# Kernel tuning notes

Measured on AMD Instinct MI355X. Metric: run time of the kernel, lower is better.

Reference implementation:

```python
import jax, jax.numpy as jnp
import numpy as np

B, S, H = 64, 512, 768
N_SPANS, MAX_SPAN, CW = 4, 8, 3
NH = 8
HD = H // NH
W = MAX_SPAN + 1 + 2 * CW  # max context window length (15)
H2 = H // 2
N_ATE, N_SENT = 2, 2


def _ln(x, g, b, eps=1e-5):
    m = x.mean(-1, keepdims=True)
    v = ((x - m) ** 2).mean(-1, keepdims=True)
    return (x - m) / jnp.sqrt(v + eps) * g + b


def _classifier(x, w1, b1, g, bb, w2, b2):
    # Dropout -> Linear -> GELU -> LayerNorm -> Linear (eval mode: dropout = id)
    h = jax.nn.gelu(x @ w1.T + b1, approximate=False)
    h = _ln(h, g, bb)
    return h @ w2.T + b2


def setup_inputs() -> dict:
    key = jax.random.key(0)
    ks = jax.random.split(key, 16)
    p = lambda k, shape: (0.02 * jax.random.normal(k, shape)).astype(jnp.float32)
    seq_out = jax.random.normal(ks[0], (B, S, H), dtype=jnp.float32)
    starts = jax.random.randint(ks[1], (B, N_SPANS), 1, S - MAX_SPAN - 1)
    lens = jax.random.randint(ks[2], (B, N_SPANS), 1, MAX_SPAN + 1)
    ends = starts + lens  # exclusive end, span length in [1, MAX_SPAN]
    return dict(
        seq_out=seq_out,
        span_starts=starts.astype(jnp.int32),
        span_ends=ends.astype(jnp.int32),
        ate_g=jnp.ones((H,), jnp.float32), ate_b=jnp.zeros((H,), jnp.float32),
        apc_g=jnp.ones((H,), jnp.float32), apc_b=jnp.zeros((H,), jnp.float32),
        w_in=p(ks[3], (3 * H, H)), b_in=jnp.zeros((3 * H,), jnp.float32),
        w_out=p(ks[4], (H, H)), b_out=jnp.zeros((H,), jnp.float32),
        fus_w=p(ks[5], (H, 2 * H)), fus_b=jnp.zeros((H,), jnp.float32),
        asp_w1=p(ks[6], (H2, H)), asp_b1=jnp.zeros((H2,), jnp.float32),
        asp_lng=jnp.ones((H2,), jnp.float32), asp_lnb=jnp.zeros((H2,), jnp.float32),
        asp_w2=p(ks[7], (N_ATE, H2)), asp_b2=jnp.zeros((N_ATE,), jnp.float32),
        sen_w1=p(ks[8], (H2, H)), sen_b1=jnp.zeros((H2,), jnp.float32),
        sen_lng=jnp.ones((H2,), jnp.float32), sen_lnb=jnp.zeros((H2,), jnp.float32),
        sen_w2=p(ks[9], (N_SENT, H2)), sen_b2=jnp.zeros((N_SENT,), jnp.float32),
    )


def _fwd(seq_out, ate_g, ate_b, apc_g, apc_b, w_in, b_in, w_out, b_out,
         fus_w, fus_b, asp_w1, asp_b1, asp_lng, asp_lnb, asp_w2, asp_b2,
         sen_w1, sen_b1, sen_lng, sen_lnb, sen_w2, sen_b2,
         span_starts, span_ends):
    dt = seq_out.dtype
    # clamping semantics as in the torch loop
    s = jnp.clip(span_starts, 0, S - 1)
    e = jnp.maximum(s, jnp.minimum(span_ends, S - 1))
    left = jnp.maximum(0, s - CW)
    right = jnp.minimum(S, e + 1 + CW)

    # ATE head over all tokens
    ate_logits = _classifier(_ln(seq_out, ate_g, ate_b),
                             asp_w1, asp_b1, asp_lng, asp_lnb, asp_w2, asp_b2)

    gather = jax.vmap(lambda so, idx: so[idx])  # ([S,H],[N,W]) -> [N,W,H]

    # aspect mean over tokens [s, e)
    aidx = s[..., None] + jnp.arange(MAX_SPAN)          # [B,N,MS]
    va = (aidx < e[..., None]).astype(dt)
    asp_tok = gather(seq_out, jnp.clip(aidx, 0, S - 1)) # [B,N,MS,H]
    cnt = va.sum(-1, keepdims=True)                     # [B,N,1]
    asp_mean = (asp_tok * va[..., None]).sum(-2) / jnp.maximum(cnt, 1.0)
    asp_mean = jnp.where(cnt > 0, asp_mean, seq_out[:, None, 0, :])

    # context window [left, right): tiny self-attention, then mean
    cidx = left[..., None] + jnp.arange(W)              # [B,N,W]
    vc = (cidx < right[..., None]).astype(dt)
    ctx = gather(seq_out, jnp.clip(cidx, 0, S - 1))     # [B,N,W,H]
    qkv = ctx @ w_in.T + b_in
    q, k, v = jnp.split(qkv, 3, axis=-1)
    q = q.reshape(B, N_SPANS, W, NH, HD) * (HD ** -0.5)
    k = k.reshape(B, N_SPANS, W, NH, HD)
    v = v.reshape(B, N_SPANS, W, NH, HD)
    scores = jnp.einsum('bnqhd,bnkhd->bnhqk', q, k)
    neg = jnp.asarray(jnp.finfo(dt).min, dt)
    scores = jnp.where(vc[:, :, None, None, :] > 0, scores, neg)
    attn = jax.nn.softmax(scores, axis=-1)
    out = jnp.einsum('bnhqk,bnkhd->bnqhd', attn, v).reshape(B, N_SPANS, W, H)
    out = out @ w_out.T + b_out
    ccnt = vc.sum(-1, keepdims=True)
    ctx_mean = (out * vc[..., None]).sum(-2) / jnp.maximum(ccnt, 1.0)

    combined = jnp.concatenate([asp_mean, ctx_mean], axis=-1)  # [B,N,2H]
    fused = jax.nn.gelu(combined @ fus_w.T + fus_b, approximate=False)
    apc_feat = fused.mean(axis=1)                              # [B,H]
    apc_logits = _classifier(_ln(apc_feat, apc_g, apc_b),
                             sen_w1, sen_b1, sen_lng, sen_lnb, sen_w2, sen_b2)
    return ate_logits, apc_logits


def reference(seq_out, span_starts, span_ends, ate_g, ate_b, apc_g, apc_b,
              w_in, b_in, w_out, b_out, fus_w, fus_b,
              asp_w1, asp_b1, asp_lng, asp_lnb, asp_w2, asp_b2,
              sen_w1, sen_b1, sen_lng, sen_lnb, sen_w2, sen_b2):
    return _fwd(seq_out, ate_g, ate_b, apc_g, apc_b, w_in, b_in, w_out, b_out,
                fus_w, fus_b, asp_w1, asp_b1, asp_lng, asp_lnb, asp_w2, asp_b2,
                sen_w1, sen_b1, sen_lng, sen_lnb, sen_w2, sen_b2,
                span_starts, span_ends)
```

## Files before the change

kernel.cpp:

```cpp
#include <hip/hip_runtime.h>
#include <math.h>

#define DEVI __device__ __forceinline__

using bf16x8 = __attribute__((ext_vector_type(8))) short;
using f32x4  = __attribute__((ext_vector_type(4))) float;

DEVI float b2f(unsigned short u) {
  union { unsigned int u; float f; } x; x.u = ((unsigned int)u) << 16; return x.f;
}
DEVI unsigned short f2b(float f) {
  union { float f; unsigned int u; } x; x.f = f;
  unsigned int r = (x.u + 0x7fffu + ((x.u >> 16) & 1u)) >> 16;
  return (unsigned short)r;
}
DEVI float gelu_f(float x) { return 0.5f * x * (1.0f + erff(x * 0.70710678118654752440f)); }

DEVI void wredxor2(float& a, float& b) {
  #pragma unroll
  for (int off = 32; off; off >>= 1) {
    a += __shfl_xor(a, off);
    b += __shfl_xor(b, off);
  }
}

template<int NW>
DEVI void breduce2(float& a, float& b) {
  __shared__ float buf[2 * NW];
  int lane = threadIdx.x & 63;
  int w = threadIdx.x >> 6;
  #pragma unroll
  for (int off = 32; off > 0; off >>= 1) {
    a += __shfl_down(a, off);
    b += __shfl_down(b, off);
  }
  if (lane == 0) { buf[w] = a; buf[NW + w] = b; }
  __syncthreads();
  float ra = 0.f, rb = 0.f;
  #pragma unroll
  for (int i = 0; i < NW; ++i) { ra += buf[i]; rb += buf[NW + i]; }
  a = ra; b = rb;
  __syncthreads();
}

DEVI void span_params(const int* st, const int* en, int span,
                      int& s, int& e, int& left, int& right) {
  int s0 = st[span], e0 = en[span];
  s = min(max(s0, 0), 511);
  e = max(s, min(e0, 511));
  left = max(0, s - 3);
  right = min(512, e + 4);
}

DEVI int xcd_logical(int bid, int n) {
  int q = n >> 3, r = n & 7;
  int xcd = bid & 7, idx = bid >> 3;
  return (xcd < r ? xcd * (q + 1) : r * (q + 1) + (xcd - r) * q) + idx;
}

__global__ __launch_bounds__(256) void prep_kernel(
    const float* __restrict__ s0, const float* __restrict__ s1,
    const float* __restrict__ s2, const float* __restrict__ s3,
    const float* __restrict__ s4,
    unsigned short* __restrict__ d0, unsigned short* __restrict__ d1,
    unsigned short* __restrict__ d2, unsigned short* __restrict__ d3,
    unsigned short* __restrict__ d4,
    const float* __restrict__ seq, const float* __restrict__ ate_g,
    const float* __restrict__ ate_b, unsigned short* __restrict__ lnx,
    const int* __restrict__ st, const int* __restrict__ en,
    unsigned short* __restrict__ ctxA) {
  const int bid = blockIdx.x, tid = threadIdx.x;
  if (bid < 4032) {
    int i = bid * 256 + tid;
    const float* s; unsigned short* d; int j;
    if (i < 73728)       { s = s0; d = d0; j = i; }
    else if (i < 516096) { s = s1; d = d1; j = i - 73728; }
    else if (i < 663552) { s = s2; d = d2; j = i - 516096; }
    else if (i < 958464) { s = s3; d = d3; j = i - 663552; }
    else                 { s = s4; d = d4; j = i - 958464; }
    float4 v = reinterpret_cast<const float4*>(s)[j];
    ushort4 o;
    o.x = f2b(v.x); o.y = f2b(v.y); o.z = f2b(v.z); o.w = f2b(v.w);
    reinterpret_cast<ushort4*>(d)[j] = o;
  } else if (bid < 12224) {
    const int row = (bid - 4032) * 4 + (tid >> 6);
    const int lane = tid & 63;
    const float4* xr = reinterpret_cast<const float4*>(seq + (size_t)row * 768);
    float4 v[3];
    #pragma unroll
    for (int j = 0; j < 3; ++j) v[j] = xr[j * 64 + lane];
    float s = 0.f, q = 0.f;
    #pragma unroll
    for (int j = 0; j < 3; ++j) {
      s += v[j].x + v[j].y + v[j].z + v[j].w;
      q += v[j].x * v[j].x + v[j].y * v[j].y + v[j].z * v[j].z + v[j].w * v[j].w;
    }
    wredxor2(s, q);
    float mean = s * (1.0f / 768.0f);
    float rstd = rsqrtf(q * (1.0f / 768.0f) - mean * mean + 1e-5f);
    ushort4* orow = reinterpret_cast<ushort4*>(lnx + (size_t)row * 768);
    #pragma unroll
    for (int j = 0; j < 3; ++j) {
      float4 gv = reinterpret_cast<const float4*>(ate_g)[j * 64 + lane];
      float4 bv = reinterpret_cast<const float4*>(ate_b)[j * 64 + lane];
      ushort4 o;
      o.x = f2b((v[j].x - mean) * rstd * gv.x + bv.x);
      o.y = f2b((v[j].y - mean) * rstd * gv.y + bv.y);
      o.z = f2b((v[j].z - mean) * rstd * gv.z + bv.z);
      o.w = f2b((v[j].w - mean) * rstd * gv.w + bv.w);
      orow[j * 64 + lane] = o;
    }
  } else {
    if (tid >= 192) return;
    int r = bid - 12224;
    int span = r / 15, w = r % 15;
    int s, e, left, right;
    span_params(st, en, span, s, e, left, right);
    int b = span >> 2;
    int tok = min(left + w, 511);
    const float4* src = reinterpret_cast<const float4*>(seq + ((size_t)b * 512 + tok) * 768);
    ushort4* dst = reinterpret_cast<ushort4*>(ctxA + (size_t)r * 768);
    float4 v = src[tid];
    ushort4 o;
    o.x = f2b(v.x); o.y = f2b(v.y); o.z = f2b(v.z); o.w = f2b(v.w);
    dst[tid] = o;
  }
}

template<int BM, int BN, int WM, int WN>
DEVI void gemm_body64(const unsigned short* __restrict__ A,
                      const unsigned short* __restrict__ W,
                      const float* __restrict__ bias, unsigned short* __restrict__ C,
                      int M, int N, int K, bool act, int bm, int bn,
                      unsigned short* As, unsigned short* Bs) {
  constexpr int CA = BM / 8;
  constexpr int CB = BN / 8;
  constexpr int NWC = BN / WN;
  constexpr int WAVES = (BM / WM) * NWC;
  constexpr int FM = WM / 16, FN = WN / 16;
  const int tid = threadIdx.x;
  const int lane = tid & 63;
  const int wv = tid >> 6;
  const int wr = wv / NWC, wc = wv % NWC;
  const int l16 = lane & 15, lhi = lane >> 4;
  const int srow = lane >> 3;
  const int scol = 8 * ((lane & 7) ^ srow);

  f32x4 acc[FM][FN] = {};
  const int nt = K / 64;

  for (int t = 0; t < nt; ++t) {
    const int k0 = t * 64;
    #pragma unroll
    for (int ch = wv; ch < CA; ch += WAVES)
      __builtin_amdgcn_global_load_lds(
          (const __attribute__((address_space(1))) void*)&A[(size_t)(bm + ch * 8 + srow) * K + k0 + scol],
          (__attribute__((address_space(3))) void*)&As[ch * 512], 16, 0, 0);
    #pragma unroll
    for (int ch = wv; ch < CB; ch += WAVES)
      __builtin_amdgcn_global_load_lds(
          (const __attribute__((address_space(1))) void*)&W[(size_t)(bn + ch * 8 + srow) * K + k0 + scol],
          (__attribute__((address_space(3))) void*)&Bs[ch * 512], 16, 0, 0);
    __syncthreads();
    #pragma unroll
    for (int kk = 0; kk < 2; ++kk) {
      bf16x8 af[FM], bfr[FN];
      #pragma unroll
      for (int fm = 0; fm < FM; ++fm) {
        int r = wr * WM + fm * 16 + l16;
        af[fm] = *reinterpret_cast<const bf16x8*>(&As[r * 64 + ((kk * 32 + lhi * 8) ^ ((r & 7) * 8))]);
      }
      #pragma unroll
      for (int fn = 0; fn < FN; ++fn) {
        int r = wc * WN + fn * 16 + l16;
        bfr[fn] = *reinterpret_cast<const bf16x8*>(&Bs[r * 64 + ((kk * 32 + lhi * 8) ^ ((r & 7) * 8))]);
      }
      #pragma unroll
      for (int fm = 0; fm < FM; ++fm)
        #pragma unroll
        for (int fn = 0; fn < FN; ++fn)
          acc[fm][fn] = __builtin_amdgcn_mfma_f32_16x16x32_bf16(af[fm], bfr[fn], acc[fm][fn], 0, 0, 0);
    }
    __syncthreads();
  }

  #pragma unroll
  for (int fm = 0; fm < FM; ++fm) {
    #pragma unroll
    for (int fn = 0; fn < FN; ++fn) {
      int col = bn + wc * WN + fn * 16 + l16;
      float bv = bias[col];
      #pragma unroll
      for (int i = 0; i < 4; ++i) {
        int row = bm + wr * WM + fm * 16 + lhi * 4 + i;
        float v = acc[fm][fn][i] + bv;
        if (act) v = gelu_f(v);
        C[(size_t)row * N + col] = f2b(v);
      }
    }
  }
}

template<int BM, int BN, int WM, int WN, int ACT>
__global__ __launch_bounds__(256) void gemm_swz64(
    const unsigned short* __restrict__ A, const unsigned short* __restrict__ W,
    const float* __restrict__ bias, unsigned short* __restrict__ C,
    int M, int N, int K, int nbN) {
  __shared__ __align__(16) unsigned short As[BM * 64];
  __shared__ __align__(16) unsigned short Bs[BN * 64];
  int l = xcd_logical(blockIdx.x, gridDim.x);
  int mb = l / nbN, nb = l % nbN;
  gemm_body64<BM, BN, WM, WN>(A, W, bias, C, M, N, K, ACT != 0,
                              mb * BM, nb * BN, As, Bs);
}

__global__ __launch_bounds__(512) void dual_gemm_kernel(
    const unsigned short* __restrict__ lnx, const unsigned short* __restrict__ w1b,
    const float* __restrict__ b1, unsigned short* __restrict__ hate,
    const unsigned short* __restrict__ ctxA, const unsigned short* __restrict__ winb,
    const float* __restrict__ b_in, unsigned short* __restrict__ qkv) {
  __shared__ __align__(16) unsigned short lds[384 * 64];
  if (blockIdx.x < 384) {
    int l = xcd_logical(blockIdx.x, 384);
    int mb = l / 3, nb = l % 3;
    gemm_body64<256, 128, 64, 64>(lnx, w1b, b1, hate, 32768, 384, 768, true,
                                  mb * 256, nb * 128, lds, lds + 256 * 64);
  } else {
    int bid = blockIdx.x - 384;
    int l = xcd_logical(bid, 270);
    int mb = l / 9, nb = l % 9;
    gemm_body64<128, 256, 64, 64>(ctxA, winb, b_in, qkv, 3840, 2304, 768, false,
                                  mb * 128, nb * 256, lds, lds + 128 * 64);
  }
}

__global__ __launch_bounds__(256) void finattn_kernel(
    const unsigned short* __restrict__ h, const float* __restrict__ lng,
    const float* __restrict__ lnb, const float* __restrict__ w2,
    const float* __restrict__ b2, float* __restrict__ out,
    const unsigned short* __restrict__ qkv, const int* __restrict__ st,
    const int* __restrict__ en, unsigned short* __restrict__ ctxO) {
  __shared__ float qs[15][96], ks[15][96], vs[15][96];
  __shared__ float sc[15][16];
  const int tid = threadIdx.x;
  if (blockIdx.x < 8192) {
    const int row = blockIdx.x * 4 + (tid >> 6);
    const int lane = tid & 63;
    const unsigned short* hr = h + (size_t)row * 384 + lane * 6;
    ushort2 u0 = *reinterpret_cast<const ushort2*>(hr);
    ushort2 u1 = *reinterpret_cast<const ushort2*>(hr + 2);
    ushort2 u2 = *reinterpret_cast<const ushort2*>(hr + 4);
    float v[6] = { b2f(u0.x), b2f(u0.y), b2f(u1.x), b2f(u1.y), b2f(u2.x), b2f(u2.y) };
    float s = 0.f, q = 0.f;
    #pragma unroll
    for (int j = 0; j < 6; ++j) { s += v[j]; q += v[j] * v[j]; }
    wredxor2(s, q);
    float mean = s * (1.f / 384.f);
    float rstd = rsqrtf(q * (1.f / 384.f) - mean * mean + 1e-5f);
    const int c0 = lane * 6;
    float p0 = 0.f, p1 = 0.f;
    #pragma unroll
    for (int j = 0; j < 6; ++j) {
      float hl = (v[j] - mean) * rstd * lng[c0 + j] + lnb[c0 + j];
      p0 += hl * w2[c0 + j];
      p1 += hl * w2[384 + c0 + j];
    }
    wredxor2(p0, p1);
    if (lane == 0) {
      out[(size_t)row * 2]     = p0 + b2[0];
      out[(size_t)row * 2 + 1] = p1 + b2[1];
    }
    return;
  }
  const int blk = blockIdx.x - 8192;
  const int span = blk >> 3, hh = blk & 7;
  int s, e, left, right;
  span_params(st, en, span, s, e, left, right);
  const int nv = right - left;
  const int r0 = span * 15;
  const float scale = 0.10206207261596576f;
  if (tid < 180) {
    int w = tid / 12, dp = tid % 12, d = dp * 8;
    const unsigned short* rowp = qkv + (size_t)(r0 + w) * 2304 + hh * 96 + d;
    bf16x8 qv = *reinterpret_cast<const bf16x8*>(rowp);
    bf16x8 kv = *reinterpret_cast<const bf16x8*>(rowp + 768);
    bf16x8 vv = *reinterpret_cast<const bf16x8*>(rowp + 1536);
    #pragma unroll
    for (int j = 0; j < 8; ++j) {
      qs[w][d + j] = b2f((unsigned short)qv[j]) * scale;
      ks[w][d + j] = b2f((unsigned short)kv[j]);
      vs[w][d + j] = b2f((unsigned short)vv[j]);
    }
  }
  __syncthreads();
  if (tid < 225) {
    int i = tid / 15, j = tid % 15;
    float a = 0.f;
    #pragma unroll
    for (int d = 0; d < 96; ++d) a += qs[i][d] * ks[j][d];
    sc[i][j] = (j < nv) ? a : -3.402823466e38f;
  }
  __syncthreads();
  if (tid < 15) {
    int i = tid;
    float m = -3.402823466e38f;
    #pragma unroll
    for (int j = 0; j < 15; ++j) m = fmaxf(m, sc[i][j]);
    float ex[15];
    float ssum = 0.f;
    #pragma unroll
    for (int j = 0; j < 15; ++j) { ex[j] = expf(sc[i][j] - m); ssum += ex[j]; }
    float inv = 1.0f / ssum;
    #pragma unroll
    for (int j = 0; j < 15; ++j) sc[i][j] = ex[j] * inv;
  }
  __syncthreads();
  for (int idx = tid; idx < 720; idx += 256) {
    int w = idx / 48, dp = idx % 48, d = dp * 2;
    float o0 = 0.f, o1 = 0.f;
    #pragma unroll
    for (int j = 0; j < 15; ++j) {
      float p = sc[w][j];
      o0 += p * vs[j][d];
      o1 += p * vs[j][d + 1];
    }
    ushort2 o; o.x = f2b(o0); o.y = f2b(o1);
    *reinterpret_cast<ushort2*>(&ctxO[(size_t)(r0 + w) * 768 + hh * 96 + d]) = o;
  }
}

__global__ __launch_bounds__(256) void means_kernel(
    const float* __restrict__ seq, const unsigned short* __restrict__ projO,
    const int* __restrict__ st, const int* __restrict__ en,
    unsigned short* __restrict__ comb) {
  const int span = blockIdx.x;
  int s, e, left, right;
  span_params(st, en, span, s, e, left, right);
  int b = span >> 2;
  int e2 = min(e, s + 8);
  int cnt = e2 - s;
  int nv = right - left;
  float inva = (cnt > 0) ? 1.0f / (float)cnt : 0.f;
  float invc = 1.0f / (float)nv;
  for (int c = threadIdx.x; c < 768; c += 256) {
    float sa = 0.f;
    for (int t = s; t < e2; ++t) sa += seq[((size_t)b * 512 + t) * 768 + c];
    float asp = (cnt > 0) ? sa * inva : seq[((size_t)b * 512) * 768 + c];
    comb[(size_t)span * 1536 + c] = f2b(asp);
    float sc_ = 0.f;
    for (int w = 0; w < nv; ++w) sc_ += b2f(projO[(size_t)(span * 15 + w) * 768 + c]);
    comb[(size_t)span * 1536 + 768 + c] = f2b(sc_ * invc);
  }
}

__global__ __launch_bounds__(256) void apc_all_kernel(
    const unsigned short* __restrict__ fused, const float* __restrict__ g,
    const float* __restrict__ bb, const unsigned short* __restrict__ senb,
    const float* __restrict__ b1, const float* __restrict__ lng,
    const float* __restrict__ lnb, const float* __restrict__ w2,
    const float* __restrict__ b2, float* __restrict__ out) {
  const int b = blockIdx.x, tid = threadIdx.x;
  __shared__ float xs[768];
  __shared__ float hs[384];
  float v[3];
  #pragma unroll
  for (int j = 0; j < 3; ++j) {
    int c = tid + j * 256;
    float a = 0.f;
    #pragma unroll
    for (int n = 0; n < 4; ++n) a += b2f(fused[((size_t)(b * 4 + n)) * 768 + c]);
    v[j] = 0.25f * a;
  }
  float s = v[0] + v[1] + v[2];
  float q = v[0] * v[0] + v[1] * v[1] + v[2] * v[2];
  breduce2<4>(s, q);
  float mean = s * (1.f / 768.f);
  float rstd = rsqrtf(q * (1.f / 768.f) - mean * mean + 1e-5f);
  #pragma unroll
  for (int j = 0; j < 3; ++j) {
    int c = tid + j * 256;
    xs[c] = (v[j] - mean) * rstd * g[c] + bb[c];
  }
  __syncthreads();
  for (int j = tid; j < 384; j += 256) {
    const bf16x8* wrp = reinterpret_cast<const bf16x8*>(senb + (size_t)j * 768);
    float dot = 0.f;
    #pragma unroll 4
    for (int k8 = 0; k8 < 96; ++k8) {
      bf16x8 wv = wrp[k8];
      #pragma unroll
      for (int u = 0; u < 8; ++u) dot += xs[k8 * 8 + u] * b2f((unsigned short)wv[u]);
    }
    hs[j] = gelu_f(dot + b1[j]);
  }
  __syncthreads();
  s = 0.f; q = 0.f;
  for (int j = tid; j < 384; j += 256) { float h = hs[j]; s += h; q += h * h; }
  breduce2<4>(s, q);
  mean = s * (1.f / 384.f);
  rstd = rsqrtf(q * (1.f / 384.f) - mean * mean + 1e-5f);
  float p0 = 0.f, p1 = 0.f;
  for (int j = tid; j < 384; j += 256) {
    float hl = (hs[j] - mean) * rstd * lng[j] + lnb[j];
    p0 += hl * w2[j];
    p1 += hl * w2[384 + j];
  }
  breduce2<4>(p0, p1);
  if (tid == 0) {
    out[b * 2]     = p0 + b2[0];
    out[b * 2 + 1] = p1 + b2[1];
  }
}

extern "C" void kernel_launch(void* const* d_in, const int* in_sizes, int n_in,
                              void* d_out, int out_size, void* d_ws, size_t ws_size,
                              hipStream_t stream) {
  const float* seq    = (const float*)d_in[0];
  const int*   st     = (const int*)d_in[1];
  const int*   en     = (const int*)d_in[2];
  const float* ate_g  = (const float*)d_in[3];
  const float* ate_b  = (const float*)d_in[4];
  const float* apc_g  = (const float*)d_in[5];
  const float* apc_b  = (const float*)d_in[6];
  const float* w_in   = (const float*)d_in[7];
  const float* b_in   = (const float*)d_in[8];
  const float* w_out  = (const float*)d_in[9];
  const float* b_out  = (const float*)d_in[10];
  const float* fus_w  = (const float*)d_in[11];
  const float* fus_b  = (const float*)d_in[12];
  const float* asp_w1 = (const float*)d_in[13];
  const float* asp_b1 = (const float*)d_in[14];
  const float* asp_lng= (const float*)d_in[15];
  const float* asp_lnb= (const float*)d_in[16];
  const float* asp_w2 = (const float*)d_in[17];
  const float* asp_b2 = (const float*)d_in[18];
  const float* sen_w1 = (const float*)d_in[19];
  const float* sen_b1 = (const float*)d_in[20];
  const float* sen_lng= (const float*)d_in[21];
  const float* sen_lnb= (const float*)d_in[22];
  const float* sen_w2 = (const float*)d_in[23];
  const float* sen_b2 = (const float*)d_in[24];
  float* out = (float*)d_out;

  char* wsb = (char*)d_ws;
  unsigned short* lnx   = (unsigned short*)(wsb + 0);
  unsigned short* ctxA  = (unsigned short*)(wsb + 52428800);
  unsigned short* qkvb  = (unsigned short*)(wsb + 58720256);
  unsigned short* ctxO  = (unsigned short*)(wsb + 77594624);
  unsigned short* projO = (unsigned short*)(wsb + 83886080);
  unsigned short* comb  = (unsigned short*)(wsb + 89849856);
  unsigned short* fusO  = (unsigned short*)(wsb + 90636288);
  const size_t off_w = 91275264;
  unsigned short* hate  = (unsigned short*)(wsb + off_w);
  const size_t off_w2 = off_w + 25165824;
  unsigned short* w1b   = (unsigned short*)(wsb + off_w2);
  unsigned short* winb  = (unsigned short*)(wsb + off_w2 + 589824);
  unsigned short* woutb = (unsigned short*)(wsb + off_w2 + 4128768);
  unsigned short* fusb  = (unsigned short*)(wsb + off_w2 + 5308416);
  unsigned short* senb  = (unsigned short*)(wsb + off_w2 + 7667712);

  prep_kernel<<<16064, 256, 0, stream>>>(asp_w1, w_in, w_out, fus_w, sen_w1,
                                         w1b, winb, woutb, fusb, senb,
                                         seq, ate_g, ate_b, lnx, st, en, ctxA);
  dual_gemm_kernel<<<654, 512, 0, stream>>>(lnx, w1b, asp_b1, hate,
                                            ctxA, winb, b_in, qkvb);
  finattn_kernel<<<10240, 256, 0, stream>>>(hate, asp_lng, asp_lnb, asp_w2, asp_b2, out,
                                            qkvb, st, en, ctxO);
  gemm_swz64<64, 128, 32, 64, 0><<<360, 256, 0, stream>>>(
      ctxO, woutb, b_out, projO, 3840, 768, 768, 6);
  means_kernel<<<256, 256, 0, stream>>>(seq, projO, st, en, comb);
  gemm_swz64<64, 64, 32, 32, 1><<<48, 256, 0, stream>>>(
      comb, fusb, fus_b, fusO, 256, 768, 1536, 12);
  apc_all_kernel<<<64, 256, 0, stream>>>(fusO, apc_g, apc_b, senb, sen_b1,
                                         sen_lng, sen_lnb, sen_w2, sen_b2, out + 65536);
}
```

Before: 188.0 us.

## Fuse ATE LayerNorm and final projection into first GEMM epilogue via partial sums

The ATE classifier's hidden activations are no longer written out in bf16 and re-read. Instead the GEMM epilogue computes per-row partial sums, sums of squares and gamma-weighted dot products with w2, and stores them as small float4 partials. A light pass in the attention kernel then combines the partials and applies the LayerNorm algebraically to produce the logits. This removes the 32768x384 bf16 intermediate round trip and thousands of reduction blocks. The cost is extra shuffle reductions in the epilogue, plus variance computed as E[h^2]-mu^2 in fp32, which has different rounding.

Result: faster. 183.2 us (-2.5%).

```diff
diff --git a/kernel.cpp b/kernel.cpp
--- a/kernel.cpp
+++ b/kernel.cpp
@@ -128,11 +128,11 @@
 }
 
 template<int BM, int BN, int WM, int WN>
-DEVI void gemm_body64(const unsigned short* __restrict__ A,
-                      const unsigned short* __restrict__ W,
-                      const float* __restrict__ bias, unsigned short* __restrict__ C,
-                      int M, int N, int K, bool act, int bm, int bn,
-                      unsigned short* As, unsigned short* Bs) {
+DEVI void gemm_core(const unsigned short* __restrict__ A,
+                    const unsigned short* __restrict__ W,
+                    int K, int bm, int bn,
+                    unsigned short* As, unsigned short* Bs,
+                    f32x4 (&acc)[WM / 16][WN / 16]) {
   constexpr int CA = BM / 8;
   constexpr int CB = BN / 8;
   constexpr int NWC = BN / WN;
@@ -146,9 +146,7 @@
   const int srow = lane >> 3;
   const int scol = 8 * ((lane & 7) ^ srow);
 
-  f32x4 acc[FM][FN] = {};
   const int nt = K / 64;
-
   for (int t = 0; t < nt; ++t) {
     const int k0 = t * 64;
     #pragma unroll
@@ -183,7 +181,17 @@
     }
     __syncthreads();
   }
-
+}
+
+template<int BM, int BN, int WM, int WN>
+DEVI void gemm_store(const float* __restrict__ bias, unsigned short* __restrict__ C,
+                     int N, bool act, int bm, int bn, f32x4 (&acc)[WM / 16][WN / 16]) {
+  constexpr int NWC = BN / WN;
+  constexpr int FM = WM / 16, FN = WN / 16;
+  const int lane = threadIdx.x & 63;
+  const int wv = threadIdx.x >> 6;
+  const int wr = wv / NWC, wc = wv % NWC;
+  const int l16 = lane & 15, lhi = lane >> 4;
   #pragma unroll
   for (int fm = 0; fm < FM; ++fm) {
     #pragma unroll
@@ -210,70 +218,113 @@
   __shared__ __align__(16) unsigned short Bs[BN * 64];
   int l = xcd_logical(blockIdx.x, gridDim.x);
   int mb = l / nbN, nb = l % nbN;
-  gemm_body64<BM, BN, WM, WN>(A, W, bias, C, M, N, K, ACT != 0,
-                              mb * BM, nb * BN, As, Bs);
+  f32x4 acc[WM / 16][WN / 16] = {};
+  gemm_core<BM, BN, WM, WN>(A, W, K, mb * BM, nb * BN, As, Bs, acc);
+  gemm_store<BM, BN, WM, WN>(bias, C, N, ACT != 0, mb * BM, nb * BN, acc);
 }
 
 __global__ __launch_bounds__(512) void dual_gemm_kernel(
     const unsigned short* __restrict__ lnx, const unsigned short* __restrict__ w1b,
-    const float* __restrict__ b1, unsigned short* __restrict__ hate,
+    const float* __restrict__ b1, const float* __restrict__ lng,
+    const float* __restrict__ w2, float4* __restrict__ hpart,
     const unsigned short* __restrict__ ctxA, const unsigned short* __restrict__ winb,
     const float* __restrict__ b_in, unsigned short* __restrict__ qkv) {
   __shared__ __align__(16) unsigned short lds[384 * 64];
   if (blockIdx.x < 384) {
     int l = xcd_logical(blockIdx.x, 384);
     int mb = l / 3, nb = l % 3;
-    gemm_body64<256, 128, 64, 64>(lnx, w1b, b1, hate, 32768, 384, 768, true,
-                                  mb * 256, nb * 128, lds, lds + 256 * 64);
+    const int bm = mb * 256, bn = nb * 128;
+    f32x4 acc[4][4] = {};
+    gemm_core<256, 128, 64, 64>(lnx, w1b, 768, bm, bn, lds, lds + 256 * 64, acc);
+    const int lane = threadIdx.x & 63;
+    const int wv = threadIdx.x >> 6;
+    const int wr = wv >> 1, wc = wv & 1;
+    const int l16 = lane & 15, lhi = lane >> 4;
+    float b1v[4], gw2a[4], gw2b[4];
+    #pragma unroll
+    for (int fn = 0; fn < 4; ++fn) {
+      int col = bn + wc * 64 + fn * 16 + l16;
+      b1v[fn] = b1[col];
+      float gg = lng[col];
+      gw2a[fn] = gg * w2[col];
+      gw2b[fn] = gg * w2[384 + col];
+    }
+    #pragma unroll
+    for (int fm = 0; fm < 4; ++fm) {
+      #pragma unroll
+      for (int i = 0; i < 4; ++i) {
+        float s1 = 0.f, s2 = 0.f, q0 = 0.f, q1 = 0.f;
+        #pragma unroll
+        for (int fn = 0; fn < 4; ++fn) {
+          float h = gelu_f(acc[fm][fn][i] + b1v[fn]);
+          s1 += h; s2 += h * h;
+          q0 += h * gw2a[fn]; q1 += h * gw2b[fn];
+        }
+        #pragma unroll
+        for (int off = 1; off < 16; off <<= 1) {
+          s1 += __shfl_xor(s1, off); s2 += __shfl_xor(s2, off);
+          q0 += __shfl_xor(q0, off); q1 += __shfl_xor(q1, off);
+        }
+        if (l16 == 0) {
+          int row = bm + wr * 64 + fm * 16 + lhi * 4 + i;
+          hpart[(size_t)row * 6 + nb * 2 + wc] = make_float4(s1, s2, q0, q1);
+        }
+      }
+    }
   } else {
     int bid = blockIdx.x - 384;
     int l = xcd_logical(bid, 270);
     int mb = l / 9, nb = l % 9;
-    gemm_body64<128, 256, 64, 64>(ctxA, winb, b_in, qkv, 3840, 2304, 768, false,
-                                  mb * 128, nb * 256, lds, lds + 128 * 64);
+    f32x4 acc[4][4] = {};
+    gemm_core<128, 256, 64, 64>(ctxA, winb, 768, mb * 128, nb * 256,
+                                lds, lds + 128 * 64, acc);
+    gemm_store<128, 256, 64, 64>(b_in, qkv, 2304, false, mb * 128, nb * 256, acc);
   }
 }
 
 __global__ __launch_bounds__(256) void finattn_kernel(
-    const unsigned short* __restrict__ h, const float* __restrict__ lng,
+    const float4* __restrict__ hpart, const float* __restrict__ lng,
     const float* __restrict__ lnb, const float* __restrict__ w2,
     const float* __restrict__ b2, float* __restrict__ out,
     const unsigned short* __restrict__ qkv, const int* __restrict__ st,
     const int* __restrict__ en, unsigned short* __restrict__ ctxO) {
+  const int tid = threadIdx.x;
+  if (blockIdx.x >= 2048) {
+    __shared__ float cbuf[16];
+    float c1a = 0.f, c1b = 0.f, c2a = 0.f, c2b = 0.f;
+    for (int c = tid; c < 384; c += 256) {
+      float gg = lng[c], bbv = lnb[c], wa = w2[c], wb = w2[384 + c];
+      c1a += gg * wa; c1b += gg * wb;
+      c2a += bbv * wa; c2b += bbv * wb;
+    }
+    wredxor2(c1a, c1b);
+    wredxor2(c2a, c2b);
+    if ((tid & 63) == 0) {
+      int w = tid >> 6;
+      cbuf[w * 4] = c1a; cbuf[w * 4 + 1] = c1b;
+      cbuf[w * 4 + 2] = c2a; cbuf[w * 4 + 3] = c2b;
+    }
+    __syncthreads();
+    c1a = cbuf[0] + cbuf[4] + cbuf[8] + cbuf[12];
+    c1b = cbuf[1] + cbuf[5] + cbuf[9] + cbuf[13];
+    c2a = cbuf[2] + cbuf[6] + cbuf[10] + cbuf[14];
+    c2b = cbuf[3] + cbuf[7] + cbuf[11] + cbuf[15];
+    const int row = (blockIdx.x - 2048) * 256 + tid;
+    float S1 = 0.f, S2 = 0.f, D0 = 0.f, D1 = 0.f;
+    #pragma unroll
+    for (int p = 0; p < 6; ++p) {
+      float4 v = hpart[(size_t)row * 6 + p];
+      S1 += v.x; S2 += v.y; D0 += v.z; D1 += v.w;
+    }
+    float mu = S1 * (1.f / 384.f);
+    float rstd = rsqrtf(S2 * (1.f / 384.f) - mu * mu + 1e-5f);
+    out[(size_t)row * 2]     = rstd * (D0 - mu * c1a) + c2a + b2[0];
+    out[(size_t)row * 2 + 1] = rstd * (D1 - mu * c1b) + c2b + b2[1];
+    return;
+  }
   __shared__ float qs[15][96], ks[15][96], vs[15][96];
   __shared__ float sc[15][16];
-  const int tid = threadIdx.x;
-  if (blockIdx.x < 8192) {
-    const int row = blockIdx.x * 4 + (tid >> 6);
-    const int lane = tid & 63;
-    const unsigned short* hr = h + (size_t)row * 384 + lane * 6;
-    ushort2 u0 = *reinterpret_cast<const ushort2*>(hr);
-    ushort2 u1 = *reinterpret_cast<const ushort2*>(hr + 2);
-    ushort2 u2 = *reinterpret_cast<const ushort2*>(hr + 4);
-    float v[6] = { b2f(u0.x), b2f(u0.y), b2f(u1.x), b2f(u1.y), b2f(u2.x), b2f(u2.y) };
-    float s = 0.f, q = 0.f;
-    #pragma unroll
-    for (int j = 0; j < 6; ++j) { s += v[j]; q += v[j] * v[j]; }
-    wredxor2(s, q);
-    float mean = s * (1.f / 384.f);
-    float rstd = rsqrtf(q * (1.f / 384.f) - mean * mean + 1e-5f);
-    const int c0 = lane * 6;
-    float p0 = 0.f, p1 = 0.f;
-    #pragma unroll
-    for (int j = 0; j < 6; ++j) {
-      float hl = (v[j] - mean) * rstd * lng[c0 + j] + lnb[c0 + j];
-      p0 += hl * w2[c0 + j];
-      p1 += hl * w2[384 + c0 + j];
-    }
-    wredxor2(p0, p1);
-    if (lane == 0) {
-      out[(size_t)row * 2]     = p0 + b2[0];
-      out[(size_t)row * 2 + 1] = p1 + b2[1];
-    }
-    return;
-  }
-  const int blk = blockIdx.x - 8192;
-  const int span = blk >> 3, hh = blk & 7;
+  const int span = blockIdx.x >> 3, hh = blockIdx.x & 7;
   int s, e, left, right;
   span_params(st, en, span, s, e, left, right);
   const int nv = right - left;
@@ -451,7 +502,7 @@
   unsigned short* comb  = (unsigned short*)(wsb + 89849856);
   unsigned short* fusO  = (unsigned short*)(wsb + 90636288);
   const size_t off_w = 91275264;
-  unsigned short* hate  = (unsigned short*)(wsb + off_w);
+  float4*        hpart  = (float4*)(wsb + off_w);
   const size_t off_w2 = off_w + 25165824;
   unsigned short* w1b   = (unsigned short*)(wsb + off_w2);
   unsigned short* winb  = (unsigned short*)(wsb + off_w2 + 589824);
@@ -462,10 +513,10 @@
   prep_kernel<<<16064, 256, 0, stream>>>(asp_w1, w_in, w_out, fus_w, sen_w1,
                                          w1b, winb, woutb, fusb, senb,
                                          seq, ate_g, ate_b, lnx, st, en, ctxA);
-  dual_gemm_kernel<<<654, 512, 0, stream>>>(lnx, w1b, asp_b1, hate,
+  dual_gemm_kernel<<<654, 512, 0, stream>>>(lnx, w1b, asp_b1, asp_lng, asp_w2, hpart,
                                             ctxA, winb, b_in, qkvb);
-  finattn_kernel<<<10240, 256, 0, stream>>>(hate, asp_lng, asp_lnb, asp_w2, asp_b2, out,
-                                            qkvb, st, en, ctxO);
+  finattn_kernel<<<2176, 256, 0, stream>>>(hpart, asp_lng, asp_lnb, asp_w2, asp_b2, out,
+                                           qkvb, st, en, ctxO);
   gemm_swz64<64, 128, 32, 64, 0><<<360, 256, 0, stream>>>(
       ctxO, woutb, b_out, projO, 3840, 768, 768, 6);
   means_kernel<<<256, 256, 0, stream>>>(seq, projO, st, en, comb);
```
